# Optimization experiments

Measured on AMD Instinct MI355X. Metric: run time of the kernel, lower is better.

The kernel has to match this reference:

```python
import jax, jax.numpy as jnp
import numpy as np

C = 512        # concept_num
D = 256        # input_dim / embedding_dim
H = 512        # msg_hidden_dim
M = 256        # msg_output_dim
OH = 512       # hidden_dim
T = 2          # edge_type_num
E = C * (C - 1)  # fully-connected graph without self-loops = 261632


def _glorot(key, shape, fan_in):
    return jax.random.normal(key, shape, jnp.float32) / np.sqrt(fan_in).astype(np.float32)


def setup_inputs() -> dict:
    key = jax.random.key(0)
    ks = jax.random.split(key, 12)
    inputs = jax.random.normal(ks[0], (C, D), jnp.float32)
    rel_type = jax.random.uniform(ks[1], (E, T), jnp.float32)
    send_idx = jax.random.randint(ks[2], (E,), 0, C, jnp.int32)
    rec_idx = jax.random.randint(ks[3], (E,), 0, C, jnp.int32)
    # per-edge-type message MLP params, stacked over type dim
    W1 = _glorot(ks[4], (T, 2 * D, H), 2 * D)
    b1 = jnp.zeros((T, H), jnp.float32)
    W2 = _glorot(ks[5], (T, H, M), H)
    b2 = jnp.zeros((T, M), jnp.float32)
    # output MLP params
    Wo1 = _glorot(ks[6], (M, OH), M)
    bo1 = jnp.zeros((OH,), jnp.float32)
    Wo2 = _glorot(ks[7], (OH, OH), OH)
    bo2 = jnp.zeros((OH,), jnp.float32)
    Wo3 = _glorot(ks[8], (OH, D), OH)
    bo3 = jnp.zeros((D,), jnp.float32)
    return {"inputs": inputs, "rel_type": rel_type, "W1": W1, "b1": b1,
            "W2": W2, "b2": b2, "Wo1": Wo1, "bo1": bo1, "Wo2": Wo2,
            "bo2": bo2, "Wo3": Wo3, "bo3": bo3,
            "send_idx": send_idx, "rec_idx": rec_idx}


def reference(inputs, rel_type, W1, b1, W2, b2, Wo1, bo1, Wo2, bo2, Wo3, bo3,
              send_idx, rec_idx):
    # node2edge: one-hot sparse matmul == index gather
    senders = jnp.take(inputs, send_idx, axis=0)      # [E, D]
    receivers = jnp.take(inputs, rec_idx, axis=0)     # [E, D]
    pre_msg = jnp.concatenate([senders, receivers], axis=-1)  # [E, 2D]
    # per-edge-type MLPs, weighted-summed by rel_type (dropout=0 / eval mode)
    all_msgs = jnp.zeros((pre_msg.shape[0], M), jnp.float32)
    for i in range(T):
        msg = jax.nn.relu(pre_msg @ W1[i] + b1[i])    # [E, H]
        msg = jax.nn.relu(msg @ W2[i] + b2[i])        # [E, M]
        all_msgs = all_msgs + msg * rel_type[:, i:i + 1]
    # edge2node: transposed one-hot sparse matmul == scatter-add over receivers
    agg_msgs = jax.ops.segment_sum(all_msgs, rec_idx, num_segments=inputs.shape[0])  # [C, M]
    pred = jax.nn.relu(agg_msgs @ Wo1 + bo1)
    pred = jax.nn.relu(pred @ Wo2 + bo2)
    return pred @ Wo3 + bo3                           # [C, D]
```

## Files before the change

kernel.cpp:

```cpp
#include <hip/hip_runtime.h>

#define C_N   512
#define E_N   261632
#define CAP   768

typedef _Float16 f16;
typedef _Float16 f16x8_t __attribute__((ext_vector_type(8)));
typedef float    f32x16_t __attribute__((ext_vector_type(16)));

__global__ __launch_bounds__(256) void k_prep_all(
    const float* __restrict__ inputs, const float* __restrict__ W1,
    const float* __restrict__ b1, const float* __restrict__ W2,
    const float* __restrict__ Wo1, const float* __restrict__ Wo2, const float* __restrict__ Wo3,
    f16* __restrict__ SA, f16* __restrict__ RB, f16* __restrict__ W2p,
    f16* __restrict__ Wo1p, f16* __restrict__ Wo2p, f16* __restrict__ Wo3p,
    int* __restrict__ cnt, float* __restrict__ agg)
{
  __shared__ f16 wt[2][256][18];
  int bid = blockIdx.x;
  int tid = threadIdx.x;
  if (bid < 64) {
    int lane = tid & 63, w = tid >> 6;
    int hlf = lane >> 5, l31 = lane & 31;
    int br = bid & 7, bc = (bid >> 3) & 1, mi = bid >> 4;
    int t = mi >> 1, half = mi & 1;
    const float* Wsrc = W1 + (size_t)t * 512 * 512 + (size_t)half * 256 * 512;

    f32x16_t acc[2][2];
    #pragma unroll
    for (int rt = 0; rt < 2; rt++)
      #pragma unroll
      for (int ctl = 0; ctl < 2; ctl++)
        #pragma unroll
        for (int r = 0; r < 16; r++) acc[rt][ctl][r] = 0.f;

    #pragma unroll
    for (int i = 0; i < 4; i++) {
      int idx = tid + i * 256;
      int k = idx >> 6, n4 = idx & 63;
      float4 v = *(const float4*)&Wsrc[(size_t)k * 512 + bc * 256 + n4 * 4];
      wt[0][n4 * 4 + 0][k] = (f16)v.x;
      wt[0][n4 * 4 + 1][k] = (f16)v.y;
      wt[0][n4 * 4 + 2][k] = (f16)v.z;
      wt[0][n4 * 4 + 3][k] = (f16)v.w;
    }

    for (int kc = 0; kc < 16; kc++) {
      __syncthreads();
      if (kc + 1 < 16) {
        int b = (kc + 1) & 1;
        #pragma unroll
        for (int i = 0; i < 4; i++) {
          int idx = tid + i * 256;
          int k = idx >> 6, n4 = idx & 63;
          float4 v = *(const float4*)&Wsrc[(size_t)((kc + 1) * 16 + k) * 512 + bc * 256 + n4 * 4];
          wt[b][n4 * 4 + 0][k] = (f16)v.x;
          wt[b][n4 * 4 + 1][k] = (f16)v.y;
          wt[b][n4 * 4 + 2][k] = (f16)v.z;
          wt[b][n4 * 4 + 3][k] = (f16)v.w;
        }
      }
      f16x8_t af[2];
      #pragma unroll
      for (int rt = 0; rt < 2; rt++) {
        const float4* p = (const float4*)&inputs[(size_t)(br * 64 + rt * 32 + l31) * 256 + kc * 16 + hlf * 8];
        float4 u0 = p[0], u1 = p[1];
        af[rt] = (f16x8_t){(f16)u0.x, (f16)u0.y, (f16)u0.z, (f16)u0.w,
                           (f16)u1.x, (f16)u1.y, (f16)u1.z, (f16)u1.w};
      }
      int b = kc & 1;
      #pragma unroll
      for (int ctl = 0; ctl < 2; ctl++) {
        int n = (2 * w + ctl) * 32 + l31;
        f16x8_t bfr = *(const f16x8_t*)&wt[b][n][hlf * 8];
        #pragma unroll
        for (int rt = 0; rt < 2; rt++)
          acc[rt][ctl] = __builtin_amdgcn_mfma_f32_32x32x16_f16(af[rt], bfr, acc[rt][ctl], 0, 0, 0);
      }
    }
    f16* dst = (half == 0) ? SA : RB;
    #pragma unroll
    for (int ctl = 0; ctl < 2; ctl++) {
      int col = bc * 256 + (2 * w + ctl) * 32 + l31;
      float bias = (half == 1) ? b1[t * 512 + col] : 0.f;
      #pragma unroll
      for (int rt = 0; rt < 2; rt++)
        #pragma unroll
        for (int r = 0; r < 16; r++) {
          int row = br * 64 + rt * 32 + (r & 3) + 8 * (r >> 2) + 4 * hlf;
          dst[((size_t)(t * 512 + row)) * 512 + col] = (f16)(acc[rt][ctl][r] + bias);
        }
    }
  } else if (bid < 192) {
    int gid  = (bid - 64) * 256 + tid;
    int lane = gid & 63;
    int ct   = (gid >> 6) & 7;
    int kc   = (gid >> 9) & 31;
    int t    = gid >> 14;
    int n    = ct * 32 + (lane & 31);
    int k0   = kc * 16 + (lane >> 5) * 8;
    const float* src = W2 + (size_t)t * 512 * 256;
    f16x8_t v;
    #pragma unroll
    for (int j = 0; j < 8; j++) v[j] = (f16)src[(size_t)(k0 + j) * 256 + n];
    *(f16x8_t*)(W2p + (size_t)gid * 8) = v;
  } else if (bid < 256) {
    int gid  = (bid - 192) * 256 + tid;
    int lane = gid & 63;
    int ct   = (gid >> 6) & 15;
    int kc   = gid >> 10;
    int n    = ct * 32 + (lane & 31);
    int k0   = kc * 16 + (lane >> 5) * 8;
    f16x8_t v;
    #pragma unroll
    for (int j = 0; j < 8; j++) v[j] = (f16)Wo1[(size_t)(k0 + j) * 512 + n];
    *(f16x8_t*)(Wo1p + (size_t)gid * 8) = v;
  } else if (bid < 384) {
    int gid  = (bid - 256) * 256 + tid;
    int lane = gid & 63;
    int ct   = (gid >> 6) & 15;
    int kc   = gid >> 10;
    int n    = ct * 32 + (lane & 31);
    int k0   = kc * 16 + (lane >> 5) * 8;
    f16x8_t v;
    #pragma unroll
    for (int j = 0; j < 8; j++) v[j] = (f16)Wo2[(size_t)(k0 + j) * 512 + n];
    *(f16x8_t*)(Wo2p + (size_t)gid * 8) = v;
  } else if (bid < 448) {
    int gid  = (bid - 384) * 256 + tid;
    int lane = gid & 63;
    int ct   = (gid >> 6) & 7;
    int kc   = gid >> 9;
    int n    = ct * 32 + (lane & 31);
    int k0   = kc * 16 + (lane >> 5) * 8;
    f16x8_t v;
    #pragma unroll
    for (int j = 0; j < 8; j++) v[j] = (f16)Wo3[(size_t)(k0 + j) * 256 + n];
    *(f16x8_t*)(Wo3p + (size_t)gid * 8) = v;
  } else if (bid == 448) {
    for (int i = tid; i < 512 * 16; i += 256) cnt[i] = 0;
  } else {
    float4* a4 = (float4*)agg;
    for (int i = tid; i < 512 * 64; i += 256) a4[i] = make_float4(0.f, 0.f, 0.f, 0.f);
  }
}

__global__ __launch_bounds__(512) void k_scatter_d(const int* __restrict__ rec,
    const int* __restrict__ send, const float* __restrict__ rel,
    int* __restrict__ cnt, uint2* __restrict__ smeta)
{
  __shared__ int lh[512];
  __shared__ int lb[512];
  int b = blockIdx.x;
  int e0 = b * (E_N / 128);
  lh[threadIdx.x] = 0;
  __syncthreads();
  for (int i = threadIdx.x; i < E_N / 128; i += 512)
    atomicAdd(&lh[rec[e0 + i]], 1);
  __syncthreads();
  {
    int c = lh[threadIdx.x];
    lb[threadIdx.x] = c ? atomicAdd(&cnt[threadIdx.x * 16], c) : 0;
    lh[threadIdx.x] = 0;
  }
  __syncthreads();
  for (int i = threadIdx.x; i < E_N / 128; i += 512) {
    int e = e0 + i;
    int r = rec[e];
    int p = r * CAP + lb[r] + atomicAdd(&lh[r], 1);
    f16 r0 = (f16)rel[2 * (size_t)e];
    f16 r1 = (f16)rel[2 * (size_t)e + 1];
    unsigned pk = ((unsigned)__builtin_bit_cast(unsigned short, r1) << 16)
                |  (unsigned)__builtin_bit_cast(unsigned short, r0);
    smeta[p] = make_uint2((unsigned)send[e], pk);
  }
}

#define H1S2 264

__global__ __launch_bounds__(512, 4) void k_edges(
    const f16* __restrict__ SA, const f16* __restrict__ RB,
    const f16* __restrict__ W2p, const float* __restrict__ b2,
    const uint2* __restrict__ smeta, const int* __restrict__ cnt,
    float* __restrict__ agg)
{
  __shared__ f16   h1[128 * H1S2];
  __shared__ f16   rbs[2][512];
  __shared__ float b2s[2][256];
  __shared__ float aggL[2][256];
  __shared__ __align__(16) float relv[2][128];
  __shared__ int   sends[128];

  int c   = blockIdx.x;
  int ti  = blockIdx.y;
  int n_c = cnt[c * 16];
  if (ti * 128 >= n_c) return;

  int tid  = threadIdx.x;
  int lane = tid & 63;
  int w    = tid >> 6;
  int hlf  = lane >> 5;
  int l31  = lane & 31;
  int q5   = tid & 31;
  int rb0  = tid >> 5;
  int rg   = w >> 2;
  int cg   = w & 3;

  if (tid < 128) {
    int t = tid >> 6, qq = tid & 63;
    *(f16x8_t*)&rbs[t][qq * 8] = *(const f16x8_t*)&RB[((size_t)(t * 512 + c)) * 512 + qq * 8];
  }
  ((float*)aggL)[tid] = 0.f;
  { int t = (tid >> 8) & 1, col = tid & 255; b2s[t][col] = b2[t * 256 + col]; }

  int s0 = c * CAP + ti * 128;
  int nv = n_c - ti * 128; if (nv > 128) nv = 128;

  if (tid < 128) {
    if (tid < nv) {
      uint2 m = smeta[s0 + tid];
      sends[tid] = (int)m.x;
      relv[0][tid] = (float)__builtin_bit_cast(f16, (unsigned short)(m.y & 0xffffu));
      relv[1][tid] = (float)__builtin_bit_cast(f16, (unsigned short)(m.y >> 16));
    } else {
      sends[tid] = 0; relv[0][tid] = 0.f; relv[1][tid] = 0.f;
    }
  }
  __syncthreads();

  const f16x8_t* SAc = (const f16x8_t*)SA;
  const f16x8_t* Bp  = (const f16x8_t*)W2p;

  const f16 fz = (f16)0.f;
  const f16x8_t z8 = {fz, fz, fz, fz, fz, fz, fz, fz};

  f16x8_t g[4];
  #pragma unroll
  for (int j = 0; j < 4; j++)
    g[j] = SAc[(size_t)sends[rb0 + 16 * j] * 64 + q5];

  f32x16_t acc[2][2];

  for (int ph = 0; ph < 4; ph++) {
    int t  = ph >> 1;
    int kh = ph & 1;

    f16x8_t rbq = *(const f16x8_t*)&rbs[t][(kh * 32 + q5) * 8];
    #pragma unroll
    for (int j = 0; j < 4; j++) {
      f16x8_t sv = g[j] + rbq;
      g[j] = SAc[(size_t)(t * 512 + sends[rb0 + 16 * (j + 4)]) * 64 + kh * 32 + q5];
      sv = __builtin_elementwise_max(sv, z8);
      *(f16x8_t*)&h1[(rb0 + 16 * j) * H1S2 + q5 * 8] = sv;
    }
    #pragma unroll
    for (int j = 0; j < 4; j++) {
      f16x8_t sv = g[j] + rbq;
      sv = __builtin_elementwise_max(sv, z8);
      *(f16x8_t*)&h1[(rb0 + 16 * (j + 4)) * H1S2 + q5 * 8] = sv;
    }
    __syncthreads();

    if (kh == 0) {
      #pragma unroll
      for (int a = 0; a < 2; a++)
        #pragma unroll
        for (int b_ = 0; b_ < 2; b_++)
          #pragma unroll
          for (int r = 0; r < 16; r++) acc[a][b_][r] = 0.f;
    }

    const f16x8_t* Bw = Bp + ((size_t)((t * 32 + kh * 16) * 8 + cg * 2) * 64 + lane);

    f16x8_t bb[2][2];
    bb[0][0] = Bw[0];    bb[0][1] = Bw[64];
    bb[1][0] = Bw[512];  bb[1][1] = Bw[512 + 64];

    if (ph < 3) {
      int tn  = (ph + 1) >> 1;
      int khn = (ph + 1) & 1;
      #pragma unroll
      for (int j = 0; j < 4; j++)
        g[j] = SAc[(size_t)(tn * 512 + sends[rb0 + 16 * j]) * 64 + khn * 32 + q5];
    }

    int a0 = (rg * 64 + l31) * H1S2 + hlf * 8;
    #pragma unroll
    for (int kc = 0; kc < 16; kc++) {
      int pb = kc & 1;
      f16x8_t af0 = *(const f16x8_t*)&h1[a0 + kc * 16];
      f16x8_t af1 = *(const f16x8_t*)&h1[a0 + 32 * H1S2 + kc * 16];
      acc[0][0] = __builtin_amdgcn_mfma_f32_32x32x16_f16(af0, bb[pb][0], acc[0][0], 0, 0, 0);
      acc[0][1] = __builtin_amdgcn_mfma_f32_32x32x16_f16(af0, bb[pb][1], acc[0][1], 0, 0, 0);
      acc[1][0] = __builtin_amdgcn_mfma_f32_32x32x16_f16(af1, bb[pb][0], acc[1][0], 0, 0, 0);
      acc[1][1] = __builtin_amdgcn_mfma_f32_32x32x16_f16(af1, bb[pb][1], acc[1][1], 0, 0, 0);
      if (kc + 2 < 16) {
        bb[pb][0] = Bw[(kc + 2) * 512];
        bb[pb][1] = Bw[(kc + 2) * 512 + 64];
      }
    }

    if (kh == 1) {
      #pragma unroll
      for (int ctl = 0; ctl < 2; ctl++) {
        int col = (cg * 2 + ctl) * 32 + l31;
        float b2c = b2s[t][col];
        float csum = 0.f;
        #pragma unroll
        for (int rt = 0; rt < 2; rt++) {
          int rbase = rg * 64 + rt * 32 + 4 * hlf;
          #pragma unroll
          for (int grp = 0; grp < 4; grp++) {
            float4 rv = *(const float4*)&relv[t][rbase + 8 * grp];
            float v0 = fmaxf(acc[rt][ctl][grp * 4 + 0] + b2c, 0.f);
            float v1 = fmaxf(acc[rt][ctl][grp * 4 + 1] + b2c, 0.f);
            float v2 = fmaxf(acc[rt][ctl][grp * 4 + 2] + b2c, 0.f);
            float v3 = fmaxf(acc[rt][ctl][grp * 4 + 3] + b2c, 0.f);
            csum += v0 * rv.x + v1 * rv.y + v2 * rv.z + v3 * rv.w;
          }
        }
        csum += __shfl_xor(csum, 32, 64);
        if (hlf == 0) aggL[rg][col] += csum;
      }
    }
    __syncthreads();
  }

  if (tid < 256) atomicAdd(&agg[(size_t)c * 256 + tid], aggL[0][tid] + aggL[1][tid]);
}

#define HOS 520

__global__ __launch_bounds__(512, 1) void k_omlp(const float* __restrict__ agg,
    const f16* __restrict__ Wo1p, const float* __restrict__ bo1,
    const f16* __restrict__ Wo2p, const float* __restrict__ bo2,
    const f16* __restrict__ Wo3p, const float* __restrict__ bo3,
    float* __restrict__ out)
{
  __shared__ f16 hL1[32 * HOS];
  __shared__ f16 hL2[32 * HOS];
  int tid = threadIdx.x, lane = tid & 63, w = tid >> 6;
  int hlf = lane >> 5, l31 = lane & 31;
  int br = blockIdx.x;

  {
    f32x16_t acc[2];
    #pragma unroll
    for (int ctl = 0; ctl < 2; ctl++)
      #pragma unroll
      for (int r = 0; r < 16; r++) acc[ctl][r] = 0.f;
    for (int kc = 0; kc < 16; kc++) {
      const float4* p = (const float4*)&agg[(size_t)(br * 32 + l31) * 256 + kc * 16 + hlf * 8];
      float4 u0 = p[0], u1 = p[1];
      f16x8_t af = (f16x8_t){(f16)u0.x, (f16)u0.y, (f16)u0.z, (f16)u0.w,
                             (f16)u1.x, (f16)u1.y, (f16)u1.z, (f16)u1.w};
      #pragma unroll
      for (int ctl = 0; ctl < 2; ctl++) {
        int ct = 2 * w + ctl;
        f16x8_t bfr = *(const f16x8_t*)&Wo1p[((size_t)(kc * 16 + ct) * 64 + lane) * 8];
        acc[ctl] = __builtin_amdgcn_mfma_f32_32x32x16_f16(af, bfr, acc[ctl], 0, 0, 0);
      }
    }
    #pragma unroll
    for (int ctl = 0; ctl < 2; ctl++) {
      int col = (2 * w + ctl) * 32 + l31;
      float bias = bo1[col];
      #pragma unroll
      for (int r = 0; r < 16; r++) {
        int row = (r & 3) + 8 * (r >> 2) + 4 * hlf;
        hL1[row * HOS + col] = (f16)fmaxf(acc[ctl][r] + bias, 0.f);
      }
    }
  }
  __syncthreads();

  {
    f32x16_t acc[2];
    #pragma unroll
    for (int ctl = 0; ctl < 2; ctl++)
      #pragma unroll
      for (int r = 0; r < 16; r++) acc[ctl][r] = 0.f;
    for (int kc = 0; kc < 32; kc++) {
      f16x8_t af = *(const f16x8_t*)&hL1[l31 * HOS + kc * 16 + hlf * 8];
      #pragma unroll
      for (int ctl = 0; ctl < 2; ctl++) {
        int ct = 2 * w + ctl;
        f16x8_t bfr = *(const f16x8_t*)&Wo2p[((size_t)(kc * 16 + ct) * 64 + lane) * 8];
        acc[ctl] = __builtin_amdgcn_mfma_f32_32x32x16_f16(af, bfr, acc[ctl], 0, 0, 0);
      }
    }
    #pragma unroll
    for (int ctl = 0; ctl < 2; ctl++) {
      int col = (2 * w + ctl) * 32 + l31;
      float bias = bo2[col];
      #pragma unroll
      for (int r = 0; r < 16; r++) {
        int row = (r & 3) + 8 * (r >> 2) + 4 * hlf;
        hL2[row * HOS + col] = (f16)fmaxf(acc[ctl][r] + bias, 0.f);
      }
    }
  }
  __syncthreads();

  {
    f32x16_t acc;
    #pragma unroll
    for (int r = 0; r < 16; r++) acc[r] = 0.f;
    for (int kc = 0; kc < 32; kc++) {
      f16x8_t af  = *(const f16x8_t*)&hL2[l31 * HOS + kc * 16 + hlf * 8];
      f16x8_t bfr = *(const f16x8_t*)&Wo3p[((size_t)(kc * 8 + w) * 64 + lane) * 8];
      acc = __builtin_amdgcn_mfma_f32_32x32x16_f16(af, bfr, acc, 0, 0, 0);
    }
    int col = w * 32 + l31;
    float bias = bo3[col];
    #pragma unroll
    for (int r = 0; r < 16; r++) {
      int row = br * 32 + (r & 3) + 8 * (r >> 2) + 4 * hlf;
      out[(size_t)row * 256 + col] = acc[r] + bias;
    }
  }
}

extern "C" void kernel_launch(void* const* d_in, const int* in_sizes, int n_in,
                              void* d_out, int out_size, void* d_ws, size_t ws_size,
                              hipStream_t stream)
{
  (void)in_sizes; (void)n_in; (void)out_size; (void)ws_size;
  const float* inputs = (const float*)d_in[0];
  const float* rel    = (const float*)d_in[1];
  const float* W1     = (const float*)d_in[2];
  const float* b1     = (const float*)d_in[3];
  const float* W2     = (const float*)d_in[4];
  const float* b2     = (const float*)d_in[5];
  const float* Wo1    = (const float*)d_in[6];
  const float* bo1    = (const float*)d_in[7];
  const float* Wo2    = (const float*)d_in[8];
  const float* bo2    = (const float*)d_in[9];
  const float* Wo3    = (const float*)d_in[10];
  const float* bo3    = (const float*)d_in[11];
  const int* send_idx = (const int*)d_in[12];
  const int* rec_idx  = (const int*)d_in[13];
  float* out = (float*)d_out;

  char* ws = (char*)d_ws;
  f16*    SA    = (f16*)   (ws);
  f16*    RB    = (f16*)   (ws + (1024u << 10));
  f16*    W2p   = (f16*)   (ws + (2048u << 10));
  float*  agg   = (float*) (ws + (2560u << 10));
  int*    cnt   = (int*)   (ws + (3072u << 10));
  f16*    Wo1p  = (f16*)   (ws + (3136u << 10));
  f16*    Wo2p  = (f16*)   (ws + (3392u << 10));
  f16*    Wo3p  = (f16*)   (ws + (3904u << 10));
  uint2*  smeta = (uint2*) (ws + (4160u << 10));

  k_prep_all <<<dim3(450),    dim3(256), 0, stream>>>(inputs, W1, b1, W2, Wo1, Wo2, Wo3,
                                                      SA, RB, W2p, Wo1p, Wo2p, Wo3p, cnt, agg);
  k_scatter_d<<<dim3(128),    dim3(512), 0, stream>>>(rec_idx, send_idx, rel, cnt, smeta);
  k_edges    <<<dim3(512, 5), dim3(512), 0, stream>>>(SA, RB, W2p, b2, smeta, cnt, agg);
  k_omlp     <<<dim3(16),     dim3(512), 0, stream>>>(agg, Wo1p, bo1, Wo2p, bo2, Wo3p, bo3, out);
}
```

Before: 302.0 us.

## Double-buffer h1 tiles in k_edges, splitting K into 128-wide phases

The edge kernel now splits each edge type's 512-wide hidden K dimension into four 128-wide slices instead of two 256-wide ones. It double-buffers the h1 shared tile so the next slice's gather, add and relu are written while MFMAs consume the current buffer, needing only one barrier per phase. The aim is to overlap the SA gather latency and h1 construction with matrix work and drop one barrier per phase. It doubles the phase count, and the LDS footprint stays about the same (2x128x136 vs 128x264).

```diff
diff --git a/kernel.cpp b/kernel.cpp
--- a/kernel.cpp
+++ b/kernel.cpp
@@ -176,7 +176,7 @@
   }
 }
 
-#define H1S2 264
+#define H1S 136
 
 __global__ __launch_bounds__(512, 4) void k_edges(
     const f16* __restrict__ SA, const f16* __restrict__ RB,
@@ -184,7 +184,7 @@
     const uint2* __restrict__ smeta, const int* __restrict__ cnt,
     float* __restrict__ agg)
 {
-  __shared__ f16   h1[128 * H1S2];
+  __shared__ f16   h1[2][128][H1S];
   __shared__ f16   rbs[2][512];
   __shared__ float b2s[2][256];
   __shared__ float aggL[2][256];
@@ -201,8 +201,8 @@
   int w    = tid >> 6;
   int hlf  = lane >> 5;
   int l31  = lane & 31;
-  int q5   = tid & 31;
-  int rb0  = tid >> 5;
+  int q4   = tid & 15;
+  int rb0  = tid >> 4;
   int rg   = w >> 2;
   int cg   = w & 3;
 
@@ -234,34 +234,40 @@
   const f16 fz = (f16)0.f;
   const f16x8_t z8 = {fz, fz, fz, fz, fz, fz, fz, fz};
 
-  f16x8_t g[4];
+  int voff[4];
   #pragma unroll
   for (int j = 0; j < 4; j++)
-    g[j] = SAc[(size_t)sends[rb0 + 16 * j] * 64 + q5];
-
-  f32x16_t acc[2][2];
-
-  for (int ph = 0; ph < 4; ph++) {
-    int t  = ph >> 1;
-    int kh = ph & 1;
-
-    f16x8_t rbq = *(const f16x8_t*)&rbs[t][(kh * 32 + q5) * 8];
-    #pragma unroll
-    for (int j = 0; j < 4; j++) {
-      f16x8_t sv = g[j] + rbq;
-      g[j] = SAc[(size_t)(t * 512 + sends[rb0 + 16 * (j + 4)]) * 64 + kh * 32 + q5];
-      sv = __builtin_elementwise_max(sv, z8);
-      *(f16x8_t*)&h1[(rb0 + 16 * j) * H1S2 + q5 * 8] = sv;
-    }
+    voff[j] = sends[rb0 + 32 * j] * 64 + q4;
+
+  f16x8_t g[4];
+
+  #pragma unroll
+  for (int j = 0; j < 4; j++) g[j] = SAc[voff[j]];
+  {
+    f16x8_t rbq = *(const f16x8_t*)&rbs[0][q4 * 8];
     #pragma unroll
     for (int j = 0; j < 4; j++) {
       f16x8_t sv = g[j] + rbq;
       sv = __builtin_elementwise_max(sv, z8);
-      *(f16x8_t*)&h1[(rb0 + 16 * (j + 4)) * H1S2 + q5 * 8] = sv;
-    }
+      *(f16x8_t*)&h1[0][rb0 + 32 * j][q4 * 8] = sv;
+    }
+  }
+
+  f32x16_t acc[2][2];
+
+  for (int p = 0; p < 8; p++) {
+    int t  = p >> 2;
+    int ks = p & 3;
+    int pb = p & 1;
     __syncthreads();
 
-    if (kh == 0) {
+    if (p < 7) {
+      int off = ((p + 1) >> 2) * 32768 + ((p + 1) & 3) * 16;
+      #pragma unroll
+      for (int j = 0; j < 4; j++) g[j] = SAc[voff[j] + off];
+    }
+
+    if (ks == 0) {
       #pragma unroll
       for (int a = 0; a < 2; a++)
         #pragma unroll
@@ -270,37 +276,30 @@
           for (int r = 0; r < 16; r++) acc[a][b_][r] = 0.f;
     }
 
-    const f16x8_t* Bw = Bp + ((size_t)((t * 32 + kh * 16) * 8 + cg * 2) * 64 + lane);
+    const f16x8_t* Bw = Bp + ((size_t)((t * 32 + ks * 8) * 8 + cg * 2) * 64 + lane);
 
     f16x8_t bb[2][2];
     bb[0][0] = Bw[0];    bb[0][1] = Bw[64];
     bb[1][0] = Bw[512];  bb[1][1] = Bw[512 + 64];
 
-    if (ph < 3) {
-      int tn  = (ph + 1) >> 1;
-      int khn = (ph + 1) & 1;
-      #pragma unroll
-      for (int j = 0; j < 4; j++)
-        g[j] = SAc[(size_t)(tn * 512 + sends[rb0 + 16 * j]) * 64 + khn * 32 + q5];
-    }
-
-    int a0 = (rg * 64 + l31) * H1S2 + hlf * 8;
-    #pragma unroll
-    for (int kc = 0; kc < 16; kc++) {
-      int pb = kc & 1;
-      f16x8_t af0 = *(const f16x8_t*)&h1[a0 + kc * 16];
-      f16x8_t af1 = *(const f16x8_t*)&h1[a0 + 32 * H1S2 + kc * 16];
-      acc[0][0] = __builtin_amdgcn_mfma_f32_32x32x16_f16(af0, bb[pb][0], acc[0][0], 0, 0, 0);
-      acc[0][1] = __builtin_amdgcn_mfma_f32_32x32x16_f16(af0, bb[pb][1], acc[0][1], 0, 0, 0);
-      acc[1][0] = __builtin_amdgcn_mfma_f32_32x32x16_f16(af1, bb[pb][0], acc[1][0], 0, 0, 0);
-      acc[1][1] = __builtin_amdgcn_mfma_f32_32x32x16_f16(af1, bb[pb][1], acc[1][1], 0, 0, 0);
-      if (kc + 2 < 16) {
-        bb[pb][0] = Bw[(kc + 2) * 512];
-        bb[pb][1] = Bw[(kc + 2) * 512 + 64];
-      }
-    }
-
-    if (kh == 1) {
+    const f16* h1b = &h1[pb][0][0];
+    int a0 = (rg * 64 + l31) * H1S + hlf * 8;
+    #pragma unroll
+    for (int kc = 0; kc < 8; kc++) {
+      int qb = kc & 1;
+      f16x8_t af0 = *(const f16x8_t*)&h1b[a0 + kc * 16];
+      f16x8_t af1 = *(const f16x8_t*)&h1b[a0 + 32 * H1S + kc * 16];
+      acc[0][0] = __builtin_amdgcn_mfma_f32_32x32x16_f16(af0, bb[qb][0], acc[0][0], 0, 0, 0);
+      acc[0][1] = __builtin_amdgcn_mfma_f32_32x32x16_f16(af0, bb[qb][1], acc[0][1], 0, 0, 0);
+      acc[1][0] = __builtin_amdgcn_mfma_f32_32x32x16_f16(af1, bb[qb][0], acc[1][0], 0, 0, 0);
+      acc[1][1] = __builtin_amdgcn_mfma_f32_32x32x16_f16(af1, bb[qb][1], acc[1][1], 0, 0, 0);
+      if (kc + 2 < 8) {
+        bb[qb][0] = Bw[(kc + 2) * 512];
+        bb[qb][1] = Bw[(kc + 2) * 512 + 64];
+      }
+    }
+
+    if (ks == 3) {
       #pragma unroll
       for (int ctl = 0; ctl < 2; ctl++) {
         int col = (cg * 2 + ctl) * 32 + l31;
@@ -323,8 +322,20 @@
         if (hlf == 0) aggL[rg][col] += csum;
       }
     }
-    __syncthreads();
-  }
+
+    if (p < 7) {
+      int tn = (p + 1) >> 2, ksn = (p + 1) & 3;
+      f16x8_t rbq = *(const f16x8_t*)&rbs[tn][ksn * 128 + q4 * 8];
+      #pragma unroll
+      for (int j = 0; j < 4; j++) {
+        f16x8_t sv = g[j] + rbq;
+        sv = __builtin_elementwise_max(sv, z8);
+        *(f16x8_t*)&h1[pb ^ 1][rb0 + 32 * j][q4 * 8] = sv;
+      }
+    }
+  }
+
+  __syncthreads();
 
   if (tid < 256) atomicAdd(&agg[(size_t)c * 256 + tid], aggL[0][tid] + aggL[1][tid]);
 }
```

Measured after the change: 299.4 us. Within noise of the previous version (-0.8%).
